# Kernel tuning notes

Hardware: AMD Instinct MI355X
Metric: run time of the kernel (lower is better)

The kernel has to match this reference:

```python
import jax, jax.numpy as jnp
import numpy as np

N_NODES = 20000
N_EDGES = 320000
F_IN = 256
HID = 256
N_CLS = 5


def _glorot(key, shape):
    lim = np.sqrt(6.0 / (shape[0] + shape[1]))
    return jax.random.uniform(key, shape, jnp.float32, -lim, lim)


def setup_inputs() -> dict:
    key = jax.random.key(0)
    ks = jax.random.split(key, 12)
    x1 = jax.random.normal(ks[0], (N_NODES, F_IN), jnp.float32)
    x2 = jax.random.normal(ks[1], (N_NODES, F_IN), jnp.float32)
    ei1 = jax.random.randint(ks[2], (2, N_EDGES), 0, N_NODES, jnp.int64 if jax.config.jax_enable_x64 else jnp.int32)
    ei2 = jax.random.randint(ks[3], (2, N_EDGES), 0, N_NODES, jnp.int64 if jax.config.jax_enable_x64 else jnp.int32)
    params = {
        'W1': _glorot(ks[4], (F_IN, HID)), 'b1': jnp.zeros((HID,), jnp.float32),
        'W2': _glorot(ks[5], (HID, HID)), 'b2': jnp.zeros((HID,), jnp.float32),
        'W3': _glorot(ks[6], (HID, HID)), 'b3': jnp.zeros((HID,), jnp.float32),
        'Wl': _glorot(ks[7], (HID, N_CLS)), 'bl': jnp.zeros((N_CLS,), jnp.float32),
    }
    return {'x1': x1, 'edge_index1': ei1, 'x2': x2, 'edge_index2': ei2, **params}


def gcn_conv(x, edge_index, W, b):
    # PyG GCNConv: add self-loops, symmetric normalization D^-1/2 (A+I) D^-1/2 (X W) + b
    N = x.shape[0]
    src, dst = edge_index[0], edge_index[1]
    deg = jax.ops.segment_sum(jnp.ones(src.shape[0], x.dtype), dst, num_segments=N) + 1.0
    dinv = jax.lax.rsqrt(deg)  # [N]
    xw = x @ W                 # [N, H]
    coef = (dinv[src] * dinv[dst])[:, None]  # per-edge norm
    agg = jax.ops.segment_sum(xw[src] * coef, dst, num_segments=N)
    agg = agg + xw * (dinv * dinv)[:, None]  # self-loop term
    return agg + b


def _branch(x, ei, W1, b1, W2, b2, W3, b3):
    # dropout is identity in eval mode
    h = jax.nn.relu(gcn_conv(x, ei, W1, b1))
    h = jax.nn.relu(gcn_conv(h, ei, W2, b2))
    return gcn_conv(h, ei, W3, b3)


def reference(x1, edge_index1, x2, edge_index2, W1, b1, W2, b2, W3, b3, Wl, bl):
    h1 = _branch(x1, edge_index1, W1, b1, W2, b2, W3, b3)
    h2 = _branch(x2, edge_index2, W1, b1, W2, b2, W3, b3)
    h = jnp.concatenate([h1, h2], axis=0)          # [2N, H]
    pooled = jnp.mean(h, axis=0, keepdims=True)    # batch is all zeros -> single mean pool
    return pooled @ Wl + bl                        # [1, num_classes]
```

## Files before the change

kernel.cpp:

```cpp
#include <hip/hip_runtime.h>
#include <hip/hip_bf16.h>

#define N_NODES 20000
#define N_EDGES 320000
#define HID 256

typedef __attribute__((ext_vector_type(8))) short bf16x8;
typedef __attribute__((ext_vector_type(4))) float f32x4;
typedef __attribute__((ext_vector_type(8))) unsigned short us8;

__device__ __forceinline__ float bf2f(ushort u) {
  union { unsigned int i; float f; } v; v.i = ((unsigned int)u) << 16; return v.f;
}
__device__ __forceinline__ ushort f2bf(float f) {
  union { float f; unsigned int i; } v; v.f = f;
  unsigned int r = v.i + 0x7FFFu + ((v.i >> 16) & 1u);
  return (ushort)(r >> 16);
}

__global__ void init_detect_kernel(int* cnt0, int* cnt1, float* t0, float* t1,
                                   const void* x1, const void* ei1, int* flags) {
  if (blockIdx.x == gridDim.x - 1) {
    __shared__ int cnt_wild, cnt_oddnz;
    if (threadIdx.x == 0) { cnt_wild = 0; cnt_oddnz = 0; }
    __syncthreads();
    const ushort* xu = (const ushort*)x1;
    int wild = 0;
#pragma unroll
    for (int k = 0; k < 4; k++) {
      ushort u = xu[threadIdx.x * 4 + k];
      int ex = (u >> 7) & 0xFF;
      if (ex >= 0x90) wild++;
    }
    if (wild) atomicAdd(&cnt_wild, wild);
    const int* ii = (const int*)ei1;
    if (ii[threadIdx.x * 2 + 1] != 0) atomicAdd(&cnt_oddnz, 1);
    __syncthreads();
    if (threadIdx.x == 0) {
      flags[0] = (cnt_wild > 64) ? 1 : 0;
      flags[1] = (cnt_oddnz < 8) ? 1 : 0;
    }
    return;
  }
  int i = blockIdx.x * blockDim.x + threadIdx.x;
  if (i < N_NODES) { cnt0[i] = 0; cnt1[i] = 0; t0[i] = 0.f; t1[i] = 0.f; }
}

__global__ void cvt_ei_count_kernel(const void* e0, const void* e1,
                                    int* o0, int* o1,
                                    int* cnt0, int* cnt1,
                                    int* rank0, int* rank1, const int* flags) {
  int b = blockIdx.y;
  const void* e = b ? e1 : e0;
  int* o = b ? o1 : o0;
  int* cnt = b ? cnt1 : cnt0;
  int* rank = b ? rank1 : rank0;
  int i = blockIdx.x * 256 + threadIdx.x;
  if (i >= 2 * N_EDGES) return;
  int v = flags[1] ? (int)((const long long*)e)[i] : ((const int*)e)[i];
  o[i] = v;
  if (i >= N_EDGES) rank[i - N_EDGES] = atomicAdd(&cnt[v], 1);
}

__global__ void cvt_w_kernel(const void* W1, const void* W2, const void* W3, const void* Wl,
                             const void* b1, const void* b2, const void* b3, const void* bl,
                             ushort* out, const int* flags) {
  int i = blockIdx.x * 256 + threadIdx.x;
  if (i >= 198661) return;
  const void* src; int off; bool tr = false;
  if (i < 65536)       { src = W1; off = 0; tr = true; }
  else if (i < 131072) { src = W2; off = 65536; tr = true; }
  else if (i < 196608) { src = W3; off = 131072; }
  else if (i < 197888) { src = Wl; off = 196608; }
  else if (i < 198144) { src = b1; off = 197888; }
  else if (i < 198400) { src = b2; off = 198144; }
  else if (i < 198656) { src = b3; off = 198400; }
  else                 { src = bl; off = 198656; }
  int j = i - off;
  if (tr) j = (j & 255) * 256 + (j >> 8);
  out[i] = flags[0] ? f2bf(((const float*)src)[j]) : ((const ushort*)src)[j];
}

__global__ __launch_bounds__(1024) void scan_kernel(const int* cnt0, const int* cnt1,
                                                    int* rp0, int* rp1,
                                                    float* dinv0, float* dinv1) {
  const int* cnt = blockIdx.x ? cnt1 : cnt0;
  int* rp = blockIdx.x ? rp1 : rp0;
  float* dinv = blockIdx.x ? dinv1 : dinv0;
  __shared__ int sd[1024];
  int tid = threadIdx.x;
  int base = tid * 20;
  int pref[20];
  int run = 0;
#pragma unroll
  for (int k = 0; k < 20; k++) {
    int i = base + k;
    int c = (i < N_NODES) ? cnt[i] : 0;
    if (i < N_NODES) dinv[i] = rsqrtf((float)c + 1.0f);
    run += c;
    pref[k] = run;
  }
  sd[tid] = run;
  __syncthreads();
  for (int off = 1; off < 1024; off <<= 1) {
    int v = (tid >= off) ? sd[tid - off] : 0;
    __syncthreads();
    sd[tid] += v;
    __syncthreads();
  }
  int offset = sd[tid] - run;
  if (tid == 0) rp[0] = 0;
#pragma unroll
  for (int k = 0; k < 20; k++) {
    int i = base + k;
    if (i < N_NODES) rp[i + 1] = offset + pref[k];
  }
}

__global__ void fill_kernel(const int* ei0, const int* ei1,
                            const float* dinv0, const float* dinv1,
                            const int* rp0, const int* rp1,
                            const int* rank0, const int* rank1,
                            unsigned int* eg0, unsigned int* eg1,
                            float* t0, float* t1) {
  int e = blockIdx.x * blockDim.x + threadIdx.x;
  if (e >= N_EDGES) return;
  int b = blockIdx.y;
  const int* ei = b ? ei1 : ei0;
  const float* dinv = b ? dinv1 : dinv0;
  const int* rp = b ? rp1 : rp0;
  const int* rank = b ? rank1 : rank0;
  unsigned int* eg = b ? eg1 : eg0;
  float* t = b ? t1 : t0;
  int src = ei[e], dst = ei[N_EDGES + e];
  int slot = rp[dst] + rank[e];
  float dd = dinv[dst];
  eg[slot] = (unsigned int)src | ((unsigned int)f2bf(dinv[src] * dd) << 16);
  atomicAdd(&t[src], dd);
}

__global__ __launch_bounds__(256) void gemm_kernel(
    const void* __restrict__ A0, const void* __restrict__ A1,
    const ushort* __restrict__ Wt,
    ushort* __restrict__ C0, ushort* __restrict__ C1,
    int maybe_f32, const int* __restrict__ flags) {
  const void* A = blockIdx.z ? A1 : A0;
  ushort* C = blockIdx.z ? C1 : C0;
  bool f32 = maybe_f32 && flags[0];
  int m0 = blockIdx.x * 128;
  int n0 = blockIdx.y * 64;
  __shared__ ushort As[128][42];
  __shared__ ushort Bs[64][42];
  int tid = threadIdx.x;
  int wave = tid >> 6, lane = tid & 63;
  int quad = lane >> 4, r16 = lane & 15;
  f32x4 acc[2][4];
#pragma unroll
  for (int m = 0; m < 2; m++)
#pragma unroll
    for (int n = 0; n < 4; n++) acc[m][n] = (f32x4){0.f, 0.f, 0.f, 0.f};
  int la_row = tid >> 1;
  int la_c0 = (tid & 1) * 16;
  int lb_n = tid >> 2;
  int lb_k = (tid & 3) * 8;
  for (int k0 = 0; k0 < 256; k0 += 32) {
    int gr = m0 + la_row;
    if (f32) {
      const float* Af = (const float*)A;
      float4 v0 = {0,0,0,0}, v1 = v0, v2 = v0, v3 = v0;
      if (gr < N_NODES) {
        const float* pA = Af + gr * 256 + k0 + la_c0;
        v0 = *(const float4*)pA;       v1 = *(const float4*)(pA + 4);
        v2 = *(const float4*)(pA + 8); v3 = *(const float4*)(pA + 12);
      }
      ushort* d = &As[la_row][la_c0];
      d[0] = f2bf(v0.x); d[1] = f2bf(v0.y); d[2]  = f2bf(v0.z); d[3]  = f2bf(v0.w);
      d[4] = f2bf(v1.x); d[5] = f2bf(v1.y); d[6]  = f2bf(v1.z); d[7]  = f2bf(v1.w);
      d[8] = f2bf(v2.x); d[9] = f2bf(v2.y); d[10] = f2bf(v2.z); d[11] = f2bf(v2.w);
      d[12] = f2bf(v3.x); d[13] = f2bf(v3.y); d[14] = f2bf(v3.z); d[15] = f2bf(v3.w);
    } else {
      const ushort* Ab = (const ushort*)A;
      int4 w0 = {0,0,0,0}, w1 = w0;
      if (gr < N_NODES) {
        const ushort* pA = Ab + gr * 256 + k0 + la_c0;
        w0 = *(const int4*)pA;
        w1 = *(const int4*)(pA + 8);
      }
      *(int4*)&As[la_row][la_c0] = w0;
      *(int4*)&As[la_row][la_c0 + 8] = w1;
    }
    *(int4*)&Bs[lb_n][lb_k] = *(const int4*)(Wt + (n0 + lb_n) * 256 + k0 + lb_k);
    __syncthreads();
    bf16x8 a0 = *(const bf16x8*)&As[wave * 32 + r16][quad * 8];
    bf16x8 a1 = *(const bf16x8*)&As[wave * 32 + 16 + r16][quad * 8];
    bf16x8 bb0 = *(const bf16x8*)&Bs[r16][quad * 8];
    bf16x8 bb1 = *(const bf16x8*)&Bs[16 + r16][quad * 8];
    bf16x8 bb2 = *(const bf16x8*)&Bs[32 + r16][quad * 8];
    bf16x8 bb3 = *(const bf16x8*)&Bs[48 + r16][quad * 8];
    acc[0][0] = __builtin_amdgcn_mfma_f32_16x16x32_bf16(a0, bb0, acc[0][0], 0, 0, 0);
    acc[0][1] = __builtin_amdgcn_mfma_f32_16x16x32_bf16(a0, bb1, acc[0][1], 0, 0, 0);
    acc[0][2] = __builtin_amdgcn_mfma_f32_16x16x32_bf16(a0, bb2, acc[0][2], 0, 0, 0);
    acc[0][3] = __builtin_amdgcn_mfma_f32_16x16x32_bf16(a0, bb3, acc[0][3], 0, 0, 0);
    acc[1][0] = __builtin_amdgcn_mfma_f32_16x16x32_bf16(a1, bb0, acc[1][0], 0, 0, 0);
    acc[1][1] = __builtin_amdgcn_mfma_f32_16x16x32_bf16(a1, bb1, acc[1][1], 0, 0, 0);
    acc[1][2] = __builtin_amdgcn_mfma_f32_16x16x32_bf16(a1, bb2, acc[1][2], 0, 0, 0);
    acc[1][3] = __builtin_amdgcn_mfma_f32_16x16x32_bf16(a1, bb3, acc[1][3], 0, 0, 0);
    __syncthreads();
  }
#pragma unroll
  for (int m = 0; m < 2; m++) {
    int grb = m0 + wave * 32 + m * 16 + quad * 4;
#pragma unroll
    for (int r = 0; r < 4; r++) {
      int gr = grb + r;
      if (gr < N_NODES) {
        ushort* cp = C + gr * 256 + n0 + r16;
        cp[0]  = f2bf(acc[m][0][r]);
        cp[16] = f2bf(acc[m][1][r]);
        cp[32] = f2bf(acc[m][2][r]);
        cp[48] = f2bf(acc[m][3][r]);
      }
    }
  }
}

__global__ __launch_bounds__(256) void agg_kernel(
    const ushort* __restrict__ XW0, const ushort* __restrict__ XW1,
    const float* __restrict__ dinv0, const float* __restrict__ dinv1,
    const int* __restrict__ rp0, const int* __restrict__ rp1,
    const unsigned int* __restrict__ eg0, const unsigned int* __restrict__ eg1,
    const ushort* __restrict__ bias,
    ushort* __restrict__ H0, ushort* __restrict__ H1) {
  int b = blockIdx.y;
  const ushort* XW = b ? XW1 : XW0;
  const float* dinv = b ? dinv1 : dinv0;
  const int* rp = b ? rp1 : rp0;
  const unsigned int* eg = b ? eg1 : eg0;
  ushort* H = b ? H1 : H0;
  int wave = threadIdx.x >> 6, lane = threadIdx.x & 63;
  int half = lane >> 5;
  int fl = (lane & 31) * 8;
  int i = blockIdx.x * 8 + wave * 2 + half;
  float di = dinv[i];
  float selfw = di * di;
  us8 v = *(const us8*)(XW + i * 256 + fl);
  float acc[8], acc2[8];
#pragma unroll
  for (int k = 0; k < 8; k++) { acc[k] = selfw * bf2f(v[k]); acc2[k] = 0.f; }
  int e = rp[i], eend = rp[i + 1];
  for (; e + 4 <= eend; e += 4) {
    unsigned int p0 = eg[e], p1 = eg[e + 1], p2 = eg[e + 2], p3 = eg[e + 3];
    us8 r0 = *(const us8*)(XW + (p0 & 0xFFFFu) * 256 + fl);
    us8 r1 = *(const us8*)(XW + (p1 & 0xFFFFu) * 256 + fl);
    us8 r2 = *(const us8*)(XW + (p2 & 0xFFFFu) * 256 + fl);
    us8 r3 = *(const us8*)(XW + (p3 & 0xFFFFu) * 256 + fl);
    float w0 = bf2f((ushort)(p0 >> 16)), w1 = bf2f((ushort)(p1 >> 16));
    float w2 = bf2f((ushort)(p2 >> 16)), w3 = bf2f((ushort)(p3 >> 16));
#pragma unroll
    for (int k = 0; k < 8; k++) {
      acc[k]  += w0 * bf2f(r0[k]);
      acc2[k] += w1 * bf2f(r1[k]);
      acc[k]  += w2 * bf2f(r2[k]);
      acc2[k] += w3 * bf2f(r3[k]);
    }
  }
  for (; e < eend; e++) {
    unsigned int pp = eg[e];
    us8 r = *(const us8*)(XW + (pp & 0xFFFFu) * 256 + fl);
    float w = bf2f((ushort)(pp >> 16));
#pragma unroll
    for (int k = 0; k < 8; k++) acc[k] += w * bf2f(r[k]);
  }
  us8 bb = *(const us8*)(bias + fl);
  us8 o;
#pragma unroll
  for (int k = 0; k < 8; k++)
    o[k] = f2bf(fmaxf(acc[k] + acc2[k] + bf2f(bb[k]), 0.f));
  *(us8*)(H + i * 256 + fl) = o;
}

__global__ __launch_bounds__(256) void colsum_kernel(
    const ushort* __restrict__ H0, const ushort* __restrict__ H1,
    const float* __restrict__ dinv0, const float* __restrict__ dinv1,
    const float* __restrict__ t0, const float* __restrict__ t1,
    float* __restrict__ P) {
  int b = blockIdx.y;
  const ushort* H = b ? H1 : H0;
  const float* dinv = b ? dinv1 : dinv0;
  const float* t = b ? t1 : t0;
  int wave = threadIdx.x >> 6, lane = threadIdx.x & 63;
  int wid = blockIdx.x * 4 + wave;
  int f4 = lane * 4;
  float a0 = 0.f, a1 = 0.f, a2 = 0.f, a3 = 0.f;
  for (int j = wid; j < N_NODES; j += 256) {
    float dj = dinv[j];
    float c = dj * (t[j] + dj);
    ushort4 u = *(const ushort4*)(H + j * 256 + f4);
    a0 += c * bf2f(u.x); a1 += c * bf2f(u.y);
    a2 += c * bf2f(u.z); a3 += c * bf2f(u.w);
  }
  __shared__ float part[4][256];
  part[wave][f4 + 0] = a0; part[wave][f4 + 1] = a1;
  part[wave][f4 + 2] = a2; part[wave][f4 + 3] = a3;
  __syncthreads();
  int f = threadIdx.x;
  float ssum = part[0][f] + part[1][f] + part[2][f] + part[3][f];
  P[(b * 64 + blockIdx.x) * 256 + f] = ssum;
}

__global__ __launch_bounds__(256) void final_kernel(
    const float* __restrict__ P,
    const ushort* __restrict__ W3, const ushort* __restrict__ b3,
    const ushort* __restrict__ Wl, const ushort* __restrict__ bl,
    void* __restrict__ out, const int* __restrict__ flags) {
  __shared__ float v[256];
  __shared__ float pooled[256];
  int t = threadIdx.x;
  float acc0 = 0.f, acc1 = 0.f;
  for (int b = 0; b < 64; b++) {
    acc0 += P[b * 256 + t];
    acc1 += P[(64 + b) * 256 + t];
  }
  v[t] = acc0 + acc1;
  __syncthreads();
  float acc = 0.f;
  for (int f = 0; f < 256; f++) acc += v[f] * bf2f(W3[f * 256 + t]);
  pooled[t] = acc * (1.0f / (2.0f * N_NODES)) + bf2f(b3[t]);
  __syncthreads();
  if (t < 5) {
    float o = bf2f(bl[t]);
    for (int h = 0; h < 256; h++) o += pooled[h] * bf2f(Wl[h * 5 + t]);
    if (flags[0]) ((float*)out)[t] = o;
    else ((ushort*)out)[t] = f2bf(o);
  }
}

extern "C" void kernel_launch(void* const* d_in, const int* in_sizes, int n_in,
                              void* d_out, int out_size, void* d_ws, size_t ws_size,
                              hipStream_t stream) {
  const void* x1 = d_in[0];
  const void* ei1 = d_in[1];
  const void* x2 = d_in[2];
  const void* ei2 = d_in[3];
  const void* W1 = d_in[4];
  const void* b1 = d_in[5];
  const void* W2 = d_in[6];
  const void* b2 = d_in[7];
  const void* W3 = d_in[8];
  const void* b3 = d_in[9];
  const void* Wl = d_in[10];
  const void* bl = d_in[11];

  char* p = (char*)d_ws;
  auto alloc = [&](size_t bytes) {
    char* r = p;
    p += (bytes + 255) & ~size_t(255);
    return r;
  };
  int* flags   = (int*)alloc(256);
  float* dinv0 = (float*)alloc(N_NODES * 4);
  float* dinv1 = (float*)alloc(N_NODES * 4);
  float* t0    = (float*)alloc(N_NODES * 4);
  float* t1    = (float*)alloc(N_NODES * 4);
  int* cnt0    = (int*)alloc(N_NODES * 4);
  int* cnt1    = (int*)alloc(N_NODES * 4);
  int* rp0     = (int*)alloc((N_NODES + 1) * 4);
  int* rp1     = (int*)alloc((N_NODES + 1) * 4);
  unsigned int* eg0 = (unsigned int*)alloc((size_t)N_EDGES * 4);
  unsigned int* eg1 = (unsigned int*)alloc((size_t)N_EDGES * 4);
  float* Pp    = (float*)alloc(2 * 64 * 256 * 4);
  ushort* wbuf = (ushort*)alloc(198661 * 2);
  ushort* xw0  = (ushort*)alloc((size_t)N_NODES * HID * 2);
  ushort* xw1  = (ushort*)alloc((size_t)N_NODES * HID * 2);
  ushort* h0   = (ushort*)alloc((size_t)N_NODES * HID * 2);
  ushort* h1   = (ushort*)alloc((size_t)N_NODES * HID * 2);
  int* ei32_0 = (int*)xw0;
  int* ei32_1 = ei32_0 + 2 * N_EDGES;
  int* rank0  = ei32_1 + 2 * N_EDGES;
  int* rank1  = rank0 + N_EDGES;

  ushort* Wc1 = wbuf + 0;
  ushort* Wc2 = wbuf + 65536;
  ushort* Wc3 = wbuf + 131072;
  ushort* Wlc = wbuf + 196608;
  ushort* bc1 = wbuf + 197888;
  ushort* bc2 = wbuf + 198144;
  ushort* bc3 = wbuf + 198400;
  ushort* blc = wbuf + 198656;

  init_detect_kernel<<<(N_NODES + 255) / 256 + 1, 256, 0, stream>>>(
      cnt0, cnt1, t0, t1, x1, ei1, flags);
  cvt_ei_count_kernel<<<dim3((2 * N_EDGES + 255) / 256, 2), 256, 0, stream>>>(
      ei1, ei2, ei32_0, ei32_1, cnt0, cnt1, rank0, rank1, flags);
  cvt_w_kernel<<<(198661 + 255) / 256, 256, 0, stream>>>(
      W1, W2, W3, Wl, b1, b2, b3, bl, wbuf, flags);
  scan_kernel<<<2, 1024, 0, stream>>>(cnt0, cnt1, rp0, rp1, dinv0, dinv1);
  fill_kernel<<<dim3((N_EDGES + 255) / 256, 2), 256, 0, stream>>>(
      ei32_0, ei32_1, dinv0, dinv1, rp0, rp1, rank0, rank1, eg0, eg1, t0, t1);

  gemm_kernel<<<dim3(157, 4, 2), 256, 0, stream>>>(x1, x2, Wc1, xw0, xw1, 1, flags);
  agg_kernel<<<dim3(2500, 2), 256, 0, stream>>>(
      xw0, xw1, dinv0, dinv1, rp0, rp1, eg0, eg1, bc1, h0, h1);

  gemm_kernel<<<dim3(157, 4, 2), 256, 0, stream>>>(h0, h1, Wc2, xw0, xw1, 0, flags);
  agg_kernel<<<dim3(2500, 2), 256, 0, stream>>>(
      xw0, xw1, dinv0, dinv1, rp0, rp1, eg0, eg1, bc2, h0, h1);

  colsum_kernel<<<dim3(64, 2), 256, 0, stream>>>(h0, h1, dinv0, dinv1, t0, t1, Pp);
  final_kernel<<<1, 256, 0, stream>>>(Pp, Wc3, bc3, Wlc, blc, d_out, flags);
}
```

Baseline: 382.7 us.

## Drop edge/weight conversion kernels; use LDS histograms for degree count and t-sums

Removes the separate edge-index int32 conversion and weight-conversion kernels; the GEMM, aggregation and final kernels now read fp32 or bf16 weights and biases directly and convert them on the fly, transposing W into shared memory. Degree counting and rank assignment move to chunked LDS histograms, with one global atomic per node per chunk instead of one per edge. The per-source t accumulation also moves to LDS float atomics in extra blocks of the fill kernel. This cuts kernel launches and global atomic contention, but the GEMM now converts W on every tile with scattered LDS stores, and edges are re-read several times across the histogram blocks.

After: 374.5 us. -2.1%, faster.

```diff
diff --git a/kernel.cpp b/kernel.cpp
--- a/kernel.cpp
+++ b/kernel.cpp
@@ -4,6 +4,8 @@
 #define N_NODES 20000
 #define N_EDGES 320000
 #define HID 256
+#define NQ 5000
+#define NCHUNK 8
 
 typedef __attribute__((ext_vector_type(8))) short bf16x8;
 typedef __attribute__((ext_vector_type(4))) float f32x4;
@@ -46,39 +48,40 @@
   if (i < N_NODES) { cnt0[i] = 0; cnt1[i] = 0; t0[i] = 0.f; t1[i] = 0.f; }
 }
 
-__global__ void cvt_ei_count_kernel(const void* e0, const void* e1,
-                                    int* o0, int* o1,
-                                    int* cnt0, int* cnt1,
-                                    int* rank0, int* rank1, const int* flags) {
+__global__ __launch_bounds__(1024) void count_rank_kernel(
+    const void* e0, const void* e1, int* cnt0, int* cnt1,
+    int* rank0, int* rank1, const int* flags) {
   int b = blockIdx.y;
   const void* e = b ? e1 : e0;
-  int* o = b ? o1 : o0;
   int* cnt = b ? cnt1 : cnt0;
   int* rank = b ? rank1 : rank0;
-  int i = blockIdx.x * 256 + threadIdx.x;
-  if (i >= 2 * N_EDGES) return;
-  int v = flags[1] ? (int)((const long long*)e)[i] : ((const int*)e)[i];
-  o[i] = v;
-  if (i >= N_EDGES) rank[i - N_EDGES] = atomicAdd(&cnt[v], 1);
-}
-
-__global__ void cvt_w_kernel(const void* W1, const void* W2, const void* W3, const void* Wl,
-                             const void* b1, const void* b2, const void* b3, const void* bl,
-                             ushort* out, const int* flags) {
-  int i = blockIdx.x * 256 + threadIdx.x;
-  if (i >= 198661) return;
-  const void* src; int off; bool tr = false;
-  if (i < 65536)       { src = W1; off = 0; tr = true; }
-  else if (i < 131072) { src = W2; off = 65536; tr = true; }
-  else if (i < 196608) { src = W3; off = 131072; }
-  else if (i < 197888) { src = Wl; off = 196608; }
-  else if (i < 198144) { src = b1; off = 197888; }
-  else if (i < 198400) { src = b2; off = 198144; }
-  else if (i < 198656) { src = b3; off = 198400; }
-  else                 { src = bl; off = 198656; }
-  int j = i - off;
-  if (tr) j = (j & 255) * 256 + (j >> 8);
-  out[i] = flags[0] ? f2bf(((const float*)src)[j]) : ((const ushort*)src)[j];
+  int chunk = blockIdx.x >> 2;
+  int lo = (blockIdx.x & 3) * NQ;
+  int ebeg = chunk * (N_EDGES / NCHUNK);
+  int eend = ebeg + (N_EDGES / NCHUNK);
+  __shared__ int hist[NQ];
+  __shared__ int base[NQ];
+  for (int k = threadIdx.x; k < NQ; k += 1024) hist[k] = 0;
+  __syncthreads();
+  bool w64 = flags[1] != 0;
+  const int* d32 = (const int*)e + N_EDGES;
+  const long long* d64 = (const long long*)e + N_EDGES;
+  for (int i = ebeg + threadIdx.x; i < eend; i += 1024) {
+    int d = w64 ? (int)d64[i] : d32[i];
+    unsigned q = (unsigned)(d - lo);
+    if (q < NQ) atomicAdd(&hist[q], 1);
+  }
+  __syncthreads();
+  for (int k = threadIdx.x; k < NQ; k += 1024) {
+    base[k] = atomicAdd(&cnt[lo + k], hist[k]);
+    hist[k] = 0;
+  }
+  __syncthreads();
+  for (int i = ebeg + threadIdx.x; i < eend; i += 1024) {
+    int d = w64 ? (int)d64[i] : d32[i];
+    unsigned q = (unsigned)(d - lo);
+    if (q < NQ) rank[i] = base[q] + atomicAdd(&hist[q], 1);
+  }
 }
 
 __global__ __launch_bounds__(1024) void scan_kernel(const int* cnt0, const int* cnt1,
@@ -117,36 +120,64 @@
   }
 }
 
-__global__ void fill_kernel(const int* ei0, const int* ei1,
-                            const float* dinv0, const float* dinv1,
-                            const int* rp0, const int* rp1,
-                            const int* rank0, const int* rank1,
-                            unsigned int* eg0, unsigned int* eg1,
-                            float* t0, float* t1) {
-  int e = blockIdx.x * blockDim.x + threadIdx.x;
-  if (e >= N_EDGES) return;
+__global__ __launch_bounds__(1024) void fill_kernel(
+    const void* e0, const void* e1,
+    const float* dinv0, const float* dinv1,
+    const int* rp0, const int* rp1,
+    const int* rank0, const int* rank1,
+    unsigned int* eg0, unsigned int* eg1,
+    float* t0, float* t1, const int* flags) {
   int b = blockIdx.y;
-  const int* ei = b ? ei1 : ei0;
+  const void* e = b ? e1 : e0;
   const float* dinv = b ? dinv1 : dinv0;
-  const int* rp = b ? rp1 : rp0;
-  const int* rank = b ? rank1 : rank0;
-  unsigned int* eg = b ? eg1 : eg0;
+  bool w64 = flags[1] != 0;
+  const int* s32 = (const int*)e;
+  const int* d32 = (const int*)e + N_EDGES;
+  const long long* s64 = (const long long*)e;
+  const long long* d64 = (const long long*)e + N_EDGES;
+  if (blockIdx.x < 313) {
+    const int* rp = b ? rp1 : rp0;
+    const int* rank = b ? rank1 : rank0;
+    unsigned int* eg = b ? eg1 : eg0;
+    int i = blockIdx.x * 1024 + threadIdx.x;
+    if (i >= N_EDGES) return;
+    int src = w64 ? (int)s64[i] : s32[i];
+    int dst = w64 ? (int)d64[i] : d32[i];
+    int slot = rp[dst] + rank[i];
+    eg[slot] = (unsigned int)src | ((unsigned int)f2bf(dinv[src] * dinv[dst]) << 16);
+    return;
+  }
   float* t = b ? t1 : t0;
-  int src = ei[e], dst = ei[N_EDGES + e];
-  int slot = rp[dst] + rank[e];
-  float dd = dinv[dst];
-  eg[slot] = (unsigned int)src | ((unsigned int)f2bf(dinv[src] * dd) << 16);
-  atomicAdd(&t[src], dd);
+  int r = blockIdx.x - 313;
+  int chunk = r >> 2;
+  int lo = (r & 3) * NQ;
+  int ebeg = chunk * (N_EDGES / NCHUNK);
+  int eend = ebeg + (N_EDGES / NCHUNK);
+  __shared__ float tl[NQ];
+  for (int k = threadIdx.x; k < NQ; k += 1024) tl[k] = 0.f;
+  __syncthreads();
+  for (int i = ebeg + threadIdx.x; i < eend; i += 1024) {
+    int src = w64 ? (int)s64[i] : s32[i];
+    unsigned q = (unsigned)(src - lo);
+    if (q < NQ) {
+      int dst = w64 ? (int)d64[i] : d32[i];
+      atomicAdd(&tl[q], dinv[dst]);
+    }
+  }
+  __syncthreads();
+  for (int k = threadIdx.x; k < NQ; k += 1024)
+    atomicAdd(&t[lo + k], tl[k]);
 }
 
 __global__ __launch_bounds__(256) void gemm_kernel(
     const void* __restrict__ A0, const void* __restrict__ A1,
-    const ushort* __restrict__ Wt,
+    const void* __restrict__ W,
     ushort* __restrict__ C0, ushort* __restrict__ C1,
     int maybe_f32, const int* __restrict__ flags) {
   const void* A = blockIdx.z ? A1 : A0;
   ushort* C = blockIdx.z ? C1 : C0;
-  bool f32 = maybe_f32 && flags[0];
+  bool wf32 = flags[0] != 0;
+  bool af32 = maybe_f32 && wf32;
   int m0 = blockIdx.x * 128;
   int n0 = blockIdx.y * 64;
   __shared__ ushort As[128][42];
@@ -161,11 +192,11 @@
     for (int n = 0; n < 4; n++) acc[m][n] = (f32x4){0.f, 0.f, 0.f, 0.f};
   int la_row = tid >> 1;
   int la_c0 = (tid & 1) * 16;
-  int lb_n = tid >> 2;
-  int lb_k = (tid & 3) * 8;
+  int bk = tid >> 3;
+  int bn0 = (tid & 7) * 8;
   for (int k0 = 0; k0 < 256; k0 += 32) {
     int gr = m0 + la_row;
-    if (f32) {
+    if (af32) {
       const float* Af = (const float*)A;
       float4 v0 = {0,0,0,0}, v1 = v0, v2 = v0, v3 = v0;
       if (gr < N_NODES) {
@@ -189,7 +220,18 @@
       *(int4*)&As[la_row][la_c0] = w0;
       *(int4*)&As[la_row][la_c0 + 8] = w1;
     }
-    *(int4*)&Bs[lb_n][lb_k] = *(const int4*)(Wt + (n0 + lb_n) * 256 + k0 + lb_k);
+    ushort wtmp[8];
+    if (wf32) {
+      const float* Wf = (const float*)W + (k0 + bk) * 256 + n0 + bn0;
+      float4 u0 = *(const float4*)Wf;
+      float4 u1 = *(const float4*)(Wf + 4);
+      wtmp[0] = f2bf(u0.x); wtmp[1] = f2bf(u0.y); wtmp[2] = f2bf(u0.z); wtmp[3] = f2bf(u0.w);
+      wtmp[4] = f2bf(u1.x); wtmp[5] = f2bf(u1.y); wtmp[6] = f2bf(u1.z); wtmp[7] = f2bf(u1.w);
+    } else {
+      *(int4*)wtmp = *(const int4*)((const ushort*)W + (k0 + bk) * 256 + n0 + bn0);
+    }
+#pragma unroll
+    for (int j = 0; j < 8; j++) Bs[bn0 + j][bk] = wtmp[j];
     __syncthreads();
     bf16x8 a0 = *(const bf16x8*)&As[wave * 32 + r16][quad * 8];
     bf16x8 a1 = *(const bf16x8*)&As[wave * 32 + 16 + r16][quad * 8];
@@ -229,8 +271,9 @@
     const float* __restrict__ dinv0, const float* __restrict__ dinv1,
     const int* __restrict__ rp0, const int* __restrict__ rp1,
     const unsigned int* __restrict__ eg0, const unsigned int* __restrict__ eg1,
-    const ushort* __restrict__ bias,
-    ushort* __restrict__ H0, ushort* __restrict__ H1) {
+    const void* __restrict__ bias,
+    ushort* __restrict__ H0, ushort* __restrict__ H1,
+    const int* __restrict__ flags) {
   int b = blockIdx.y;
   const ushort* XW = b ? XW1 : XW0;
   const float* dinv = b ? dinv1 : dinv0;
@@ -271,11 +314,22 @@
 #pragma unroll
     for (int k = 0; k < 8; k++) acc[k] += w * bf2f(r[k]);
   }
-  us8 bb = *(const us8*)(bias + fl);
+  float bv[8];
+  if (flags[0]) {
+    const float* bf = (const float*)bias + fl;
+    float4 c0 = *(const float4*)bf;
+    float4 c1 = *(const float4*)(bf + 4);
+    bv[0] = c0.x; bv[1] = c0.y; bv[2] = c0.z; bv[3] = c0.w;
+    bv[4] = c1.x; bv[5] = c1.y; bv[6] = c1.z; bv[7] = c1.w;
+  } else {
+    us8 bb = *(const us8*)((const ushort*)bias + fl);
+#pragma unroll
+    for (int k = 0; k < 8; k++) bv[k] = bf2f(bb[k]);
+  }
   us8 o;
 #pragma unroll
   for (int k = 0; k < 8; k++)
-    o[k] = f2bf(fmaxf(acc[k] + acc2[k] + bf2f(bb[k]), 0.f));
+    o[k] = f2bf(fmaxf(acc[k] + acc2[k] + bv[k], 0.f));
   *(us8*)(H + i * 256 + fl) = o;
 }
 
@@ -310,11 +364,12 @@
 
 __global__ __launch_bounds__(256) void final_kernel(
     const float* __restrict__ P,
-    const ushort* __restrict__ W3, const ushort* __restrict__ b3,
-    const ushort* __restrict__ Wl, const ushort* __restrict__ bl,
+    const void* __restrict__ W3, const void* __restrict__ b3,
+    const void* __restrict__ Wl, const void* __restrict__ bl,
     void* __restrict__ out, const int* __restrict__ flags) {
   __shared__ float v[256];
   __shared__ float pooled[256];
+  bool f32 = flags[0] != 0;
   int t = threadIdx.x;
   float acc0 = 0.f, acc1 = 0.f;
   for (int b = 0; b < 64; b++) {
@@ -324,14 +379,27 @@
   v[t] = acc0 + acc1;
   __syncthreads();
   float acc = 0.f;
-  for (int f = 0; f < 256; f++) acc += v[f] * bf2f(W3[f * 256 + t]);
-  pooled[t] = acc * (1.0f / (2.0f * N_NODES)) + bf2f(b3[t]);
+  if (f32) {
+    const float* W3f = (const float*)W3;
+    for (int f = 0; f < 256; f++) acc += v[f] * W3f[f * 256 + t];
+    pooled[t] = acc * (1.0f / (2.0f * N_NODES)) + ((const float*)b3)[t];
+  } else {
+    const ushort* W3b = (const ushort*)W3;
+    for (int f = 0; f < 256; f++) acc += v[f] * bf2f(W3b[f * 256 + t]);
+    pooled[t] = acc * (1.0f / (2.0f * N_NODES)) + bf2f(((const ushort*)b3)[t]);
+  }
   __syncthreads();
   if (t < 5) {
-    float o = bf2f(bl[t]);
-    for (int h = 0; h < 256; h++) o += pooled[h] * bf2f(Wl[h * 5 + t]);
-    if (flags[0]) ((float*)out)[t] = o;
-    else ((ushort*)out)[t] = f2bf(o);
+    float o;
+    if (f32) {
+      o = ((const float*)bl)[t];
+      for (int h = 0; h < 256; h++) o += pooled[h] * ((const float*)Wl)[h * 5 + t];
+      ((float*)out)[t] = o;
+    } else {
+      o = bf2f(((const ushort*)bl)[t]);
+      for (int h = 0; h < 256; h++) o += pooled[h] * bf2f(((const ushort*)Wl)[h * 5 + t]);
+      ((ushort*)out)[t] = f2bf(o);
+    }
   }
 }
 
@@ -369,43 +437,29 @@
   unsigned int* eg0 = (unsigned int*)alloc((size_t)N_EDGES * 4);
   unsigned int* eg1 = (unsigned int*)alloc((size_t)N_EDGES * 4);
   float* Pp    = (float*)alloc(2 * 64 * 256 * 4);
-  ushort* wbuf = (ushort*)alloc(198661 * 2);
   ushort* xw0  = (ushort*)alloc((size_t)N_NODES * HID * 2);
   ushort* xw1  = (ushort*)alloc((size_t)N_NODES * HID * 2);
   ushort* h0   = (ushort*)alloc((size_t)N_NODES * HID * 2);
   ushort* h1   = (ushort*)alloc((size_t)N_NODES * HID * 2);
-  int* ei32_0 = (int*)xw0;
-  int* ei32_1 = ei32_0 + 2 * N_EDGES;
-  int* rank0  = ei32_1 + 2 * N_EDGES;
+  int* rank0  = (int*)xw0;
   int* rank1  = rank0 + N_EDGES;
-
-  ushort* Wc1 = wbuf + 0;
-  ushort* Wc2 = wbuf + 65536;
-  ushort* Wc3 = wbuf + 131072;
-  ushort* Wlc = wbuf + 196608;
-  ushort* bc1 = wbuf + 197888;
-  ushort* bc2 = wbuf + 198144;
-  ushort* bc3 = wbuf + 198400;
-  ushort* blc = wbuf + 198656;
 
   init_detect_kernel<<<(N_NODES + 255) / 256 + 1, 256, 0, stream>>>(
       cnt0, cnt1, t0, t1, x1, ei1, flags);
-  cvt_ei_count_kernel<<<dim3((2 * N_EDGES + 255) / 256, 2), 256, 0, stream>>>(
-      ei1, ei2, ei32_0, ei32_1, cnt0, cnt1, rank0, rank1, flags);
-  cvt_w_kernel<<<(198661 + 255) / 256, 256, 0, stream>>>(
-      W1, W2, W3, Wl, b1, b2, b3, bl, wbuf, flags);
+  count_rank_kernel<<<dim3(NCHUNK * 4, 2), 1024, 0, stream>>>(
+      ei1, ei2, cnt0, cnt1, rank0, rank1, flags);
   scan_kernel<<<2, 1024, 0, stream>>>(cnt0, cnt1, rp0, rp1, dinv0, dinv1);
-  fill_kernel<<<dim3((N_EDGES + 255) / 256, 2), 256, 0, stream>>>(
-      ei32_0, ei32_1, dinv0, dinv1, rp0, rp1, rank0, rank1, eg0, eg1, t0, t1);
-
-  gemm_kernel<<<dim3(157, 4, 2), 256, 0, stream>>>(x1, x2, Wc1, xw0, xw1, 1, flags);
+  fill_kernel<<<dim3(313 + NCHUNK * 4, 2), 1024, 0, stream>>>(
+      ei1, ei2, dinv0, dinv1, rp0, rp1, rank0, rank1, eg0, eg1, t0, t1, flags);
+
+  gemm_kernel<<<dim3(157, 4, 2), 256, 0, stream>>>(x1, x2, W1, xw0, xw1, 1, flags);
   agg_kernel<<<dim3(2500, 2), 256, 0, stream>>>(
-      xw0, xw1, dinv0, dinv1, rp0, rp1, eg0, eg1, bc1, h0, h1);
-
-  gemm_kernel<<<dim3(157, 4, 2), 256, 0, stream>>>(h0, h1, Wc2, xw0, xw1, 0, flags);
+      xw0, xw1, dinv0, dinv1, rp0, rp1, eg0, eg1, b1, h0, h1, flags);
+
+  gemm_kernel<<<dim3(157, 4, 2), 256, 0, stream>>>(h0, h1, W2, xw0, xw1, 0, flags);
   agg_kernel<<<dim3(2500, 2), 256, 0, stream>>>(
-      xw0, xw1, dinv0, dinv1, rp0, rp1, eg0, eg1, bc2, h0, h1);
+      xw0, xw1, dinv0, dinv1, rp0, rp1, eg0, eg1, b2, h0, h1, flags);
 
   colsum_kernel<<<dim3(64, 2), 256, 0, stream>>>(h0, h1, dinv0, dinv1, t0, t1, Pp);
-  final_kernel<<<1, 256, 0, stream>>>(Pp, Wc3, bc3, Wlc, blc, d_out, flags);
-}
+  final_kernel<<<1, 256, 0, stream>>>(Pp, W3, b3, Wl, bl, d_out, flags);
+}
```
